# Optimization experiments

Hardware: AMD Instinct MI355X
Metric: run time of the kernel (lower is better)

## Reference

```python
import jax, jax.numpy as jnp
import numpy as np

N_LEADS = 12
N_HEADS = 4
LN_EPS = 1e-5

def _ecg_adj_norm():
    # Fixed 12-lead ECG adjacency with self loops, symmetric GCN normalization
    conns = [(0,1),(0,2),(1,2),(0,3),(1,3),(2,3),(0,4),(1,4),(1,5),(2,5),
             (6,7),(7,8),(8,9),(9,10),(10,11),(0,6),(1,9),(2,11)]
    A = np.zeros((N_LEADS, N_LEADS), dtype=np.float32)
    for i, j in conns:
        A[i, j] = 1.0
        A[j, i] = 1.0
    A += np.eye(N_LEADS, dtype=np.float32)
    d = A.sum(axis=1)
    dinv = 1.0 / np.sqrt(d)
    return jnp.asarray(dinv[:, None] * A * dinv[None, :])  # [12,12]

A_NORM = _ecg_adj_norm()

def gcn(x, W, b):
    # x: [B,12,F] -> A_norm @ (x W) + b
    return jnp.einsum('ij,bjf->bif', A_NORM, x @ W) + b

def mha(x, in_w, in_b, out_w, out_b):
    # x: [B,S,E]; torch nn.MultiheadAttention, batch_first=True
    B, S, E = x.shape
    D = E // N_HEADS
    qkv = x @ in_w.T + in_b                      # [B,S,3E]
    q, k, v = jnp.split(qkv, 3, axis=-1)
    def heads(t):
        return t.reshape(B, S, N_HEADS, D).transpose(0, 2, 1, 3)  # [B,H,S,D]
    q, k, v = heads(q), heads(k), heads(v)
    scores = jnp.einsum('bhsd,bhtd->bhst', q, k) / jnp.sqrt(jnp.float32(D))
    attn = jax.nn.softmax(scores, axis=-1)
    o = jnp.einsum('bhst,bhtd->bhsd', attn, v)   # [B,H,S,D]
    o = o.transpose(0, 2, 1, 3).reshape(B, S, E)
    return o @ out_w.T + out_b

def layer_norm(x, g, b):
    mu = x.mean(axis=-1, keepdims=True)
    var = ((x - mu) ** 2).mean(axis=-1, keepdims=True)
    return (x - mu) * jax.lax.rsqrt(var + LN_EPS) * g + b

def setup_inputs() -> dict:
    key = jax.random.key(0)
    ks = jax.random.split(key, 8)
    B, F_IN, H, OUT = 8192, 512, 256, 256
    s = lambda fan: 1.0 / np.sqrt(fan)
    return {
        'x': jax.random.normal(ks[0], (B, N_LEADS, F_IN), dtype=jnp.float32),
        'W1': jax.random.normal(ks[1], (F_IN, H), dtype=jnp.float32) * s(F_IN),
        'b1': jnp.zeros((H,), jnp.float32),
        'W2': jax.random.normal(ks[2], (H, H), dtype=jnp.float32) * s(H),
        'b2': jnp.zeros((H,), jnp.float32),
        'W3': jax.random.normal(ks[3], (H, OUT), dtype=jnp.float32) * s(H),
        'b3': jnp.zeros((OUT,), jnp.float32),
        'in_proj_w': jax.random.normal(ks[4], (3 * H, H), dtype=jnp.float32) * s(H),
        'in_proj_b': jnp.zeros((3 * H,), jnp.float32),
        'out_proj_w': jax.random.normal(ks[5], (H, H), dtype=jnp.float32) * s(H),
        'out_proj_b': jnp.zeros((H,), jnp.float32),
        'ln_g': jnp.ones((H,), jnp.float32),
        'ln_b': jnp.zeros((H,), jnp.float32),
    }

def reference(x, W1, b1, W2, b2, W3, b3, in_proj_w, in_proj_b, out_proj_w, out_proj_b, ln_g, ln_b):
    h = jax.nn.relu(gcn(x, W1, b1))              # dropout is identity at eval
    h = jax.nn.relu(gcn(h, W2, b2))              # [B,12,H]
    att = mha(h, in_proj_w, in_proj_b, out_proj_w, out_proj_b)
    h = layer_norm(h + att, ln_g, ln_b)
    h3 = gcn(h, W3, b3)                          # [B,12,OUT]
    w = jax.nn.softmax(h3.mean(axis=-1), axis=1) # [B,12] attention pooling
    x_weighted = jnp.einsum('bno,bn->bo', h3, w)
    x_max = h3.max(axis=1)
    return jnp.concatenate([x_weighted, x_max], axis=1)  # [B, 2*OUT]
```

## Files before the change

### kernel.cpp

```cpp
#include <hip/hip_runtime.h>
#include <hip/hip_bf16.h>
#include <cstdint>
#include <cstddef>

typedef unsigned short u16;
typedef u16 u16x8 __attribute__((ext_vector_type(8)));
typedef u16 u16x4 __attribute__((ext_vector_type(4)));
typedef __bf16 bf16x8 __attribute__((ext_vector_type(8)));
typedef float f32x4 __attribute__((ext_vector_type(4)));

__device__ const unsigned short ADJ_MASK[12] = {
    95u, 575u, 2095u, 15u, 19u, 38u, 193u, 448u, 896u, 1794u, 3584u, 3076u};

__device__ __forceinline__ float b2f(u16 u) {
  union { unsigned int i; float f; } v;
  v.i = ((unsigned int)u) << 16;
  return v.f;
}
__device__ __forceinline__ u16 f2b(float f) {
  union { float f; unsigned int i; } v;
  v.f = f;
  unsigned int r = v.i + 0x7fffu + ((v.i >> 16) & 1u);
  return (u16)(r >> 16);
}

__device__ __forceinline__ void build_anorm(float* An) {
  int t = threadIdx.x;
  if (t < 144) {
    int i = t / 12, j = t % 12;
    float di = (float)__popc((int)ADJ_MASK[i]);
    float dj = (float)__popc((int)ADJ_MASK[j]);
    An[t] = ((ADJ_MASK[i] >> j) & 1) ? (1.0f / sqrtf(di * dj)) : 0.0f;
  }
}

__global__ void __launch_bounds__(256) k_detect2(const void* a, const void* b,
                                                 int* flags) {
  const unsigned int* w = (const unsigned int*)(blockIdx.x ? b : a);
  __shared__ int s;
  if (threadIdx.x == 0) s = 0;
  __syncthreads();
  int cnt = 0;
  for (int t = 0; t < 16; ++t) {
    unsigned int v = w[t * 256 + threadIdx.x];
    unsigned int e = (v >> 7) & 0xFFu;
    if (e != 0u && (e < 0x5Au || e > 0x89u)) ++cnt;
  }
  atomicAdd(&s, cnt);
  __syncthreads();
  if (threadIdx.x == 0) flags[blockIdx.x] = (s > 1024) ? 1 : 0;
}

__global__ void __launch_bounds__(256) k_cvt_small(
    const void* b1, const void* b2, const void* b3, const void* inb,
    const void* outb, const void* lng, const void* lnb, u16* dst,
    const int* flag) {
  int idx = blockIdx.x * 256 + threadIdx.x;
  if (idx >= 2304) return;
  const void* src;
  int off = idx;
  if (idx < 256)       { src = b1; }
  else if (idx < 512)  { src = b2;   off = idx - 256; }
  else if (idx < 768)  { src = b3;   off = idx - 512; }
  else if (idx < 1536) { src = inb;  off = idx - 768; }
  else if (idx < 1792) { src = outb; off = idx - 1536; }
  else if (idx < 2048) { src = lng;  off = idx - 1792; }
  else                 { src = lnb;  off = idx - 2048; }
  dst[idx] = (*flag) ? f2b(((const float*)src)[off]) : ((const u16*)src)[off];
}

__global__ void __launch_bounds__(256) k_cvt_w(const void* inw,
                                               const void* outw, u16* dst,
                                               const int* flag) {
  int idx = blockIdx.x * 256 + threadIdx.x;
  const void* src = (idx < 196608) ? inw : outw;
  int off = (idx < 196608) ? idx : idx - 196608;
  dst[idx] = (*flag) ? f2b(((const float*)src)[off]) : ((const u16*)src)[off];
}

__global__ void __launch_bounds__(256) k_transpose3(const void* W1,
                                                    const void* W2,
                                                    const void* W3, u16* dst,
                                                    const int* flag) {
  int idx = blockIdx.x * 256 + threadIdx.x;
  const void* src;
  int R, C, li = idx;
  if (idx < 131072)      { src = W1; R = 512; C = 256; }
  else if (idx < 196608) { src = W2; R = 256; C = 256; li = idx - 131072; }
  else                   { src = W3; R = 256; C = 256; li = idx - 196608; }
  int c = li / R, r = li - c * R;
  u16 v = (*flag) ? f2b(((const float*)src)[r * C + c])
                  : ((const u16*)src)[r * C + c];
  dst[(idx - li) + c * R + r] = v;
}

__global__ void __launch_bounds__(256) k_mix(const u16* __restrict__ in,
                                             const u16* __restrict__ bias,
                                             u16* __restrict__ out, int relu) {
  __shared__ u16 X[6144];
  __shared__ float An[144];
  build_anorm(An);
  const int tid = threadIdx.x;
  const long base = (long)blockIdx.x * 6144;
#pragma unroll
  for (int i = 0; i < 3; ++i) {
    int idx = i * 256 + tid;
    *(u16x8*)(X + idx * 8) = *(const u16x8*)(in + base + idx * 8);
  }
  __syncthreads();
#pragma unroll
  for (int v = 0; v < 3; ++v) {
    int idx = v * 256 + tid;
    int s = idx / 384;
    int rem = idx - s * 384;
    int i = rem >> 5;
    int fg = rem & 31;
    float a[8];
#pragma unroll
    for (int u = 0; u < 8; ++u) a[u] = b2f(bias[fg * 8 + u]);
    for (int j = 0; j < 12; ++j) {
      float c = An[i * 12 + j];
      if (c != 0.0f) {
        u16x8 y = *(const u16x8*)(X + (s * 12 + j) * 256 + fg * 8);
#pragma unroll
        for (int u = 0; u < 8; ++u) a[u] += c * b2f(y[u]);
      }
    }
    u16x8 o;
#pragma unroll
    for (int u = 0; u < 8; ++u) {
      float vv = relu ? fmaxf(a[u], 0.0f) : a[u];
      o[u] = f2b(vv);
    }
    *(u16x8*)(out + base + idx * 8) = o;
  }
}

__device__ __forceinline__ void gemm_core(const void* __restrict__ A, int lda,
                                          int isf32,
                                          const u16* __restrict__ Bt,
                                          u16* As, u16* Bs,
                                          long m0, long n0, int K,
                                          f32x4 acc[6][4]) {
  const int tid = threadIdx.x;
  const int wave = tid >> 6, lane = tid & 63;
  const int q = lane >> 4, r16 = lane & 15;
  f32x4 zero = {0.f, 0.f, 0.f, 0.f};
#pragma unroll
  for (int a = 0; a < 6; ++a)
#pragma unroll
    for (int b = 0; b < 4; ++b) acc[a][b] = zero;

  for (int k0 = 0; k0 < K; k0 += 64) {
    if (isf32) {
      const float* Af = (const float*)A;
#pragma unroll
      for (int i = 0; i < 3; ++i) {
        int idx = i * 256 + tid;
        int rr = idx >> 3, cg = idx & 7;
        const float* sp = Af + (m0 + rr) * (long)lda + k0 + cg * 8;
        u16x8 t;
#pragma unroll
        for (int u = 0; u < 8; ++u) t[u] = f2b(sp[u]);
        *(u16x8*)(As + rr * 72 + cg * 8) = t;
      }
    } else {
      const u16* Ab = (const u16*)A;
#pragma unroll
      for (int i = 0; i < 3; ++i) {
        int idx = i * 256 + tid;
        int rr = idx >> 3, cg = idx & 7;
        *(u16x8*)(As + rr * 72 + cg * 8) =
            *(const u16x8*)(Ab + (m0 + rr) * (long)lda + k0 + cg * 8);
      }
    }
#pragma unroll
    for (int i = 0; i < 8; ++i) {
      int idx = i * 256 + tid;
      int rr = idx >> 3, cg = idx & 7;
      *(u16x8*)(Bs + rr * 72 + cg * 8) =
          *(const u16x8*)(Bt + (n0 + rr) * (long)K + k0 + cg * 8);
    }
    __syncthreads();
#pragma unroll
    for (int ks = 0; ks < 64; ks += 32) {
      bf16x8 af[6], bfv[4];
#pragma unroll
      for (int rb = 0; rb < 6; ++rb)
        af[rb] = *(const bf16x8*)(As + (rb * 16 + r16) * 72 + ks + q * 8);
#pragma unroll
      for (int cb = 0; cb < 4; ++cb)
        bfv[cb] = *(const bf16x8*)(Bs + ((wave * 4 + cb) * 16 + r16) * 72 + ks + q * 8);
#pragma unroll
      for (int rb = 0; rb < 6; ++rb)
#pragma unroll
        for (int cb = 0; cb < 4; ++cb)
          acc[rb][cb] = __builtin_amdgcn_mfma_f32_16x16x32_bf16(
              af[rb], bfv[cb], acc[rb][cb], 0, 0, 0);
    }
    __syncthreads();
  }
}

template <bool BIAS>
__global__ void __launch_bounds__(256, 2) k_gemm(const void* __restrict__ A,
                                                 int lda,
                                                 const u16* __restrict__ Bt,
                                                 const u16* __restrict__ bias,
                                                 u16* __restrict__ C,
                                                 int K, int Ntot,
                                                 const int* aflag) {
  __shared__ u16 As[96 * 72];
  __shared__ u16 Bs[256 * 72];
  f32x4 acc[6][4];
  const long m0 = (long)blockIdx.x * 96;
  const long n0 = (long)blockIdx.y * 256;
  int isf32 = aflag ? *aflag : 0;
  gemm_core(A, lda, isf32, Bt, As, Bs, m0, n0, K, acc);
  const int tid = threadIdx.x;
  const int wave = tid >> 6, lane = tid & 63;
  const int q = lane >> 4, r16 = lane & 15;
#pragma unroll
  for (int cb = 0; cb < 4; ++cb) {
    long col = n0 + (wave * 4 + cb) * 16 + r16;
    float bvv = BIAS ? b2f(bias[col]) : 0.0f;
#pragma unroll
    for (int rb = 0; rb < 6; ++rb) {
#pragma unroll
      for (int rr = 0; rr < 4; ++rr) {
        long row = m0 + rb * 16 + q * 4 + rr;
        C[row * (long)Ntot + col] = f2b(acc[rb][cb][rr] + bvv);
      }
    }
  }
}

__global__ void __launch_bounds__(256) k_attn(u16* __restrict__ QKV) {
  __shared__ u16 T[12 * 768];
  __shared__ float Sc[4][12][12];
  const int tid = threadIdx.x;
  const long base = (long)blockIdx.x * (12 * 768);
#pragma unroll
  for (int i = 0; i < 9; ++i) {
    int idx = i * 256 + tid;
    *(u16x4*)(T + idx * 4) = *(const u16x4*)(QKV + base + idx * 4);
  }
  __syncthreads();
  for (int p = tid; p < 576; p += 256) {
    int h = p / 144, r = p % 144, i = r / 12, j = r % 12;
    const u16* qp = T + i * 768 + h * 64;
    const u16* kp = T + j * 768 + 256 + h * 64;
    float s = 0.f;
#pragma unroll
    for (int dv = 0; dv < 8; ++dv) {
      u16x8 qv = *(const u16x8*)(qp + dv * 8);
      u16x8 kv = *(const u16x8*)(kp + dv * 8);
#pragma unroll
      for (int u = 0; u < 8; ++u) s += b2f(qv[u]) * b2f(kv[u]);
    }
    Sc[h][i][j] = s * 0.125f;
  }
  __syncthreads();
  if (tid < 48) {
    int h = tid / 12, i = tid % 12;
    float m = -1e30f;
#pragma unroll
    for (int j = 0; j < 12; ++j) m = fmaxf(m, Sc[h][i][j]);
    float e[12];
    float ssum = 0.f;
#pragma unroll
    for (int j = 0; j < 12; ++j) {
      e[j] = __expf(Sc[h][i][j] - m);
      ssum += e[j];
    }
    float inv = 1.0f / ssum;
#pragma unroll
    for (int j = 0; j < 12; ++j) Sc[h][i][j] = e[j] * inv;
  }
  __syncthreads();
  {
    int h = tid >> 6;
    int d = tid & 63;
    float vv[12];
#pragma unroll
    for (int j = 0; j < 12; ++j) vv[j] = b2f(T[j * 768 + 512 + h * 64 + d]);
#pragma unroll
    for (int i = 0; i < 12; ++i) {
      float o = 0.f;
#pragma unroll
      for (int j = 0; j < 12; ++j) o += Sc[h][i][j] * vv[j];
      QKV[base + i * 768 + h * 64 + d] = f2b(o);
    }
  }
}

__global__ void __launch_bounds__(256) k_resid_ln_mix(
    const u16* __restrict__ H, const u16* __restrict__ Oa,
    const u16* __restrict__ g, const u16* __restrict__ bb,
    u16* __restrict__ out) {
  __shared__ float Xn[12 * 256];
  __shared__ float An[144];
  __shared__ float mu[12], rs[12];
  build_anorm(An);
  const int tid = threadIdx.x;
  const long baseH = (long)blockIdx.x * 3072;
  const long baseO = (long)blockIdx.x * 9216;
#pragma unroll
  for (int i = 0; i < 3; ++i) {
    int idx = i * 256 + tid;
    int row = idx >> 6, c4 = idx & 63;
    u16x4 hv = *(const u16x4*)(H + baseH + idx * 4);
    u16x4 ov = *(const u16x4*)(Oa + baseO + row * 768 + c4 * 4);
#pragma unroll
    for (int u = 0; u < 4; ++u) Xn[idx * 4 + u] = b2f(hv[u]) + b2f(ov[u]);
  }
  __syncthreads();
  {
    int wave = tid >> 6, lane = tid & 63;
    for (int rr = wave; rr < 12; rr += 4) {
      float s = 0.f, s2 = 0.f;
#pragma unroll
      for (int u = 0; u < 4; ++u) {
        float xv = Xn[rr * 256 + u * 64 + lane];
        s += xv;
        s2 += xv * xv;
      }
#pragma unroll
      for (int off = 32; off > 0; off >>= 1) {
        s += __shfl_down(s, off, 64);
        s2 += __shfl_down(s2, off, 64);
      }
      if (lane == 0) {
        float m = s * (1.0f / 256.0f);
        float var = s2 * (1.0f / 256.0f) - m * m;
        mu[rr] = m;
        rs[rr] = rsqrtf(var + 1e-5f);
      }
    }
  }
  __syncthreads();
  {
    float gv = b2f(g[tid]);
    float bv = b2f(bb[tid]);
    float xn[12];
#pragma unroll
    for (int i = 0; i < 12; ++i) {
      float x = Xn[i * 256 + tid];
      xn[i] = (x - mu[i]) * rs[i] * gv + bv;
    }
#pragma unroll
    for (int i = 0; i < 12; ++i) {
      float o = 0.f;
#pragma unroll
      for (int j = 0; j < 12; ++j) o += An[i * 12 + j] * xn[j];
      out[baseH + i * 256 + tid] = f2b(o);
    }
  }
}

__global__ void __launch_bounds__(256) k_attn_mega(
    u16* __restrict__ H, const u16* __restrict__ inw,
    const u16* __restrict__ inb, const u16* __restrict__ outw,
    const u16* __restrict__ outb, const u16* __restrict__ lng,
    const u16* __restrict__ lnb) {
  __shared__ u16 Hs[32 * 264];
  __shared__ u16 Qs[32 * 264];
  __shared__ u16 KVs[24 * 512];
  __shared__ float Sc[4][2][12][12];
  __shared__ float An[144];
  __shared__ float mu[24], rs[24];
  const int tid = threadIdx.x;
  const int wave = tid >> 6, lane = tid & 63;
  const int q = lane >> 4, r16 = lane & 15;
  build_anorm(An);
  const long base = (long)blockIdx.x * 6144;
#pragma unroll
  for (int i = 0; i < 3; ++i) {
    int idx = i * 256 + tid;
    int rr = idx >> 5, cg = idx & 31;
    *(u16x8*)(Hs + rr * 264 + cg * 8) = *(const u16x8*)(H + base + idx * 8);
  }
  {
    int rr = 24 + (tid >> 5), cg = tid & 31;
    u16x8 z = {0, 0, 0, 0, 0, 0, 0, 0};
    *(u16x8*)(Hs + rr * 264 + cg * 8) = z;
  }
  __syncthreads();
  {
    f32x4 acc[2][12];
    f32x4 zero = {0.f, 0.f, 0.f, 0.f};
#pragma unroll
    for (int rb = 0; rb < 2; ++rb)
#pragma unroll
      for (int c = 0; c < 12; ++c) acc[rb][c] = zero;
    for (int k0 = 0; k0 < 256; k0 += 32) {
      bf16x8 af[2];
#pragma unroll
      for (int rb = 0; rb < 2; ++rb)
        af[rb] = *(const bf16x8*)(Hs + (rb * 16 + r16) * 264 + k0 + q * 8);
#pragma unroll
      for (int c = 0; c < 12; ++c) {
        bf16x8 bf = *(const bf16x8*)(inw + (long)((wave * 12 + c) * 16 + r16) * 256 + k0 + q * 8);
#pragma unroll
        for (int rb = 0; rb < 2; ++rb)
          acc[rb][c] = __builtin_amdgcn_mfma_f32_16x16x32_bf16(af[rb], bf, acc[rb][c], 0, 0, 0);
      }
    }
#pragma unroll
    for (int c = 0; c < 12; ++c) {
      int col = (wave * 12 + c) * 16 + r16;
      float bv = b2f(inb[col]);
#pragma unroll
      for (int rb = 0; rb < 2; ++rb)
#pragma unroll
        for (int rr2 = 0; rr2 < 4; ++rr2) {
          int row = rb * 16 + q * 4 + rr2;
          float v = acc[rb][c][rr2] + bv;
          if (col < 256) Qs[row * 264 + col] = f2b(v);
          else if (row < 24) KVs[row * 512 + col - 256] = f2b(v);
        }
    }
  }
  __syncthreads();
  {
    int h = wave;
#pragma unroll
    for (int t = 0; t < 5; ++t) {
      int p = t * 64 + lane;
      if (p < 288) {
        int s = p / 144, r = p - s * 144, i = r / 12, j = r - i * 12;
        const u16* qp = Qs + (s * 12 + i) * 264 + h * 64;
        const u16* kp = KVs + (s * 12 + j) * 512 + h * 64;
        float dot = 0.f;
#pragma unroll
        for (int dv = 0; dv < 8; ++dv) {
          u16x8 qv = *(const u16x8*)(qp + dv * 8);
          u16x8 kv = *(const u16x8*)(kp + dv * 8);
#pragma unroll
          for (int u = 0; u < 8; ++u) dot += b2f(qv[u]) * b2f(kv[u]);
        }
        Sc[h][s][i][j] = dot * 0.125f;
      }
    }
  }
  __syncthreads();
  if (lane < 24) {
    int h = wave, s = lane / 12, i = lane - (lane / 12) * 12;
    float m = -1e30f;
#pragma unroll
    for (int j = 0; j < 12; ++j) m = fmaxf(m, Sc[h][s][i][j]);
    float e[12];
    float ssum = 0.f;
#pragma unroll
    for (int j = 0; j < 12; ++j) {
      e[j] = __expf(Sc[h][s][i][j] - m);
      ssum += e[j];
    }
    float inv = 1.0f / ssum;
#pragma unroll
    for (int j = 0; j < 12; ++j) Sc[h][s][i][j] = e[j] * inv;
  }
  __syncthreads();
  {
    int h = wave, d = lane;
    for (int si = 0; si < 24; ++si) {
      int s = si / 12;
      float o = 0.f;
#pragma unroll
      for (int j = 0; j < 12; ++j)
        o += Sc[h][s][si - s * 12][j] * b2f(KVs[(s * 12 + j) * 512 + 256 + h * 64 + d]);
      Qs[si * 264 + h * 64 + d] = f2b(o);
    }
  }
  __syncthreads();
  {
    f32x4 acc[2][4];
    f32x4 zero = {0.f, 0.f, 0.f, 0.f};
#pragma unroll
    for (int rb = 0; rb < 2; ++rb)
#pragma unroll
      for (int cb = 0; cb < 4; ++cb) acc[rb][cb] = zero;
    for (int k0 = 0; k0 < 256; k0 += 32) {
      bf16x8 af[2];
#pragma unroll
      for (int rb = 0; rb < 2; ++rb)
        af[rb] = *(const bf16x8*)(Qs + (rb * 16 + r16) * 264 + k0 + q * 8);
#pragma unroll
      for (int cb = 0; cb < 4; ++cb) {
        bf16x8 bf = *(const bf16x8*)(outw + (long)((wave * 4 + cb) * 16 + r16) * 256 + k0 + q * 8);
#pragma unroll
        for (int rb = 0; rb < 2; ++rb)
          acc[rb][cb] = __builtin_amdgcn_mfma_f32_16x16x32_bf16(af[rb], bf, acc[rb][cb], 0, 0, 0);
      }
    }
#pragma unroll
    for (int cb = 0; cb < 4; ++cb) {
      int col = (wave * 4 + cb) * 16 + r16;
      float ob = b2f(outb[col]);
#pragma unroll
      for (int rb = 0; rb < 2; ++rb)
#pragma unroll
        for (int rr2 = 0; rr2 < 4; ++rr2) {
          int row = rb * 16 + q * 4 + rr2;
          if (row < 24) {
            float x = acc[rb][cb][rr2] + ob + b2f(Hs[row * 264 + col]);
            Hs[row * 264 + col] = f2b(x);
          }
        }
    }
  }
  __syncthreads();
  {
    for (int rr2 = wave * 6; rr2 < wave * 6 + 6; ++rr2) {
      float s1 = 0.f, s2 = 0.f;
#pragma unroll
      for (int u = 0; u < 4; ++u) {
        float xv = b2f(Hs[rr2 * 264 + u * 64 + lane]);
        s1 += xv;
        s2 += xv * xv;
      }
#pragma unroll
      for (int off = 32; off > 0; off >>= 1) {
        s1 += __shfl_down(s1, off, 64);
        s2 += __shfl_down(s2, off, 64);
      }
      if (lane == 0) {
        float m = s1 * (1.0f / 256.0f);
        mu[rr2] = m;
        rs[rr2] = rsqrtf(s2 * (1.0f / 256.0f) - m * m + 1e-5f);
      }
    }
  }
  __syncthreads();
  {
    float gvv = b2f(lng[tid]);
    float bvv = b2f(lnb[tid]);
#pragma unroll
    for (int s = 0; s < 2; ++s) {
      float xn[12];
#pragma unroll
      for (int j = 0; j < 12; ++j) {
        int row = s * 12 + j;
        xn[j] = (b2f(Hs[row * 264 + tid]) - mu[row]) * rs[row] * gvv + bvv;
      }
#pragma unroll
      for (int i = 0; i < 12; ++i) {
        float o = 0.f;
#pragma unroll
        for (int j = 0; j < 12; ++j) o += An[i * 12 + j] * xn[j];
        H[base + (s * 12 + i) * 256 + tid] = f2b(o);
      }
    }
  }
}

__global__ void __launch_bounds__(256, 2) k_gemm_pool(const u16* __restrict__ A,
                                                      const u16* __restrict__ Bt,
                                                      const u16* __restrict__ bias,
                                                      float* __restrict__ out) {
  __shared__ __align__(16) char smraw[50688];
  __shared__ float rowsum[96];
  __shared__ float wsm[96];
  u16* As = (u16*)smraw;
  u16* Bs = As + 96 * 72;
  u16* Y = (u16*)smraw;
  f32x4 acc[6][4];
  const long m0 = (long)blockIdx.x * 96;
  gemm_core(A, 256, 0, Bt, As, Bs, m0, 0, 256, acc);
  const int tid = threadIdx.x;
  const int wave = tid >> 6, lane = tid & 63;
  const int q = lane >> 4, r16 = lane & 15;
#pragma unroll
  for (int cb = 0; cb < 4; ++cb) {
    int col = (wave * 4 + cb) * 16 + r16;
    float bvv = b2f(bias[col]);
#pragma unroll
    for (int rb = 0; rb < 6; ++rb)
#pragma unroll
      for (int rr = 0; rr < 4; ++rr) {
        int row = rb * 16 + q * 4 + rr;
        Y[row * 264 + col] = f2b(acc[rb][cb][rr] + bvv);
      }
  }
  __syncthreads();
  for (int row = wave; row < 96; row += 4) {
    float s = 0.f;
#pragma unroll
    for (int u = 0; u < 4; ++u) s += b2f(Y[row * 264 + u * 64 + lane]);
#pragma unroll
    for (int off = 32; off > 0; off >>= 1) s += __shfl_down(s, off, 64);
    if (lane == 0) rowsum[row] = s;
  }
  __syncthreads();
  if (tid < 8) {
    float m = -1e30f;
#pragma unroll
    for (int l = 0; l < 12; ++l) m = fmaxf(m, rowsum[tid * 12 + l]);
    float e[12];
    float ssum = 0.f;
#pragma unroll
    for (int l = 0; l < 12; ++l) {
      e[l] = __expf((rowsum[tid * 12 + l] - m) * (1.0f / 256.0f));
      ssum += e[l];
    }
    float inv = 1.0f / ssum;
#pragma unroll
    for (int l = 0; l < 12; ++l) wsm[tid * 12 + l] = e[l] * inv;
  }
  __syncthreads();
  {
    int s = tid >> 5, cg = tid & 31;
    float wa[8], mx[8];
#pragma unroll
    for (int u = 0; u < 8; ++u) {
      wa[u] = 0.f;
      mx[u] = -1e30f;
    }
#pragma unroll
    for (int l = 0; l < 12; ++l) {
      float w = wsm[s * 12 + l];
      u16x8 yv = *(const u16x8*)(Y + (s * 12 + l) * 264 + cg * 8);
#pragma unroll
      for (int u = 0; u < 8; ++u) {
        float y = b2f(yv[u]);
        wa[u] += w * y;
        mx[u] = fmaxf(mx[u], y);
      }
    }
    long ob = ((long)blockIdx.x * 8 + s) * 512;
#pragma unroll
    for (int u = 0; u < 8; ++u) {
      out[ob + cg * 8 + u] = wa[u];
      out[ob + 256 + cg * 8 + u] = mx[u];
    }
  }
}

extern "C" void kernel_launch(void* const* d_in, const int* in_sizes, int n_in,
                              void* d_out, int out_size, void* d_ws,
                              size_t ws_size, hipStream_t stream) {
  (void)in_sizes; (void)n_in; (void)out_size;
  const void* x    = d_in[0];
  const void* W1   = d_in[1];
  const void* b1   = d_in[2];
  const void* W2   = d_in[3];
  const void* b2   = d_in[4];
  const void* W3   = d_in[5];
  const void* b3   = d_in[6];
  const void* inw  = d_in[7];
  const void* inb  = d_in[8];
  const void* outw = d_in[9];
  const void* outb = d_in[10];
  const void* lng  = d_in[11];
  const void* lnb  = d_in[12];
  float* out = (float*)d_out;

  u16* ws16 = (u16*)d_ws;
  int* flags = (int*)d_ws;
  u16* W1T    = ws16 + 64;
  u16* W2T    = W1T + 131072;
  u16* W3T    = W2T + 65536;
  u16* inw_b  = W3T + 65536;
  u16* outw_b = inw_b + 196608;
  u16* b1b    = outw_b + 65536;
  u16* b2b    = b1b + 256;
  u16* b3b    = b2b + 256;
  u16* inbb   = b3b + 256;
  u16* outbb  = inbb + 768;
  u16* lngb   = outbb + 256;
  u16* lnbb   = lngb + 256;
  u16* BUF    = lnbb + 256;
  u16* QKV    = BUF + 25165824L;
  const size_t NEED_A = (size_t)(QKV + 75497472L - ws16) * 2;

  k_detect2<<<2, 256, 0, stream>>>(x, W1, flags);

  k_cvt_small<<<9, 256, 0, stream>>>(b1, b2, b3, inb, outb, lng, lnb, b1b,
                                     flags + 1);
  k_cvt_w<<<1024, 256, 0, stream>>>(inw, outw, inw_b, flags + 1);
  k_transpose3<<<1024, 256, 0, stream>>>(W1, W2, W3, W1T, flags + 1);

  k_gemm<false><<<dim3(1024, 1), 256, 0, stream>>>(x, 512, W1T, nullptr, BUF, 512, 256, flags);
  k_mix<<<4096, 256, 0, stream>>>(BUF, b1b, BUF, 1);
  k_gemm<false><<<dim3(1024, 1), 256, 0, stream>>>(BUF, 256, W2T, nullptr, BUF, 256, 256, nullptr);
  k_mix<<<4096, 256, 0, stream>>>(BUF, b2b, BUF, 1);

  if (ws_size >= NEED_A) {
    k_gemm<true><<<dim3(1024, 3), 256, 0, stream>>>(BUF, 256, inw_b, inbb, QKV, 256, 768, nullptr);
    k_attn<<<8192, 256, 0, stream>>>(QKV);
    k_gemm<true><<<dim3(1024, 1), 256, 0, stream>>>(QKV, 768, outw_b, outbb, QKV + 256, 256, 768, nullptr);
    k_resid_ln_mix<<<8192, 256, 0, stream>>>(BUF, QKV + 256, lngb, lnbb, BUF);
  } else {
    k_attn_mega<<<4096, 256, 0, stream>>>(BUF, inw_b, inbb, outw_b, outbb, lngb, lnbb);
  }
  k_gemm_pool<<<1024, 256, 0, stream>>>(BUF, W3T, b3b, out);
}
```

Baseline: 688.5 us.

## Load GEMM tiles directly into LDS with XOR-swizzled layout

Replaces the register-staged global-to-LDS copies of the bf16 A and B tiles with direct global_load_lds transfers of 16 bytes per lane. The padded 72-element row stride becomes an unpadded 64-element row with XOR swizzling of 16-byte chunks to avoid bank conflicts, and the fragment reads are updated to match. This removes the VGPR round trip and shrinks LDS use. The f32 input path still goes through registers, and correctness depends on the hardware support for 16-byte direct LDS loads and on the swizzle matching between writer and reader.

```diff
diff --git a/kernel.cpp b/kernel.cpp
--- a/kernel.cpp
+++ b/kernel.cpp
@@ -23,6 +23,11 @@
   unsigned int r = v.i + 0x7fffu + ((v.i >> 16) & 1u);
   return (u16)(r >> 16);
 }
+
+#define GLOAD_LDS16(gsrc, ldst)                                         \
+  __builtin_amdgcn_global_load_lds(                                     \
+      (const __attribute__((address_space(1))) unsigned int*)(gsrc),    \
+      (__attribute__((address_space(3))) unsigned int*)(ldst), 16, 0, 0)
 
 __device__ __forceinline__ void build_anorm(float* An) {
   int t = threadIdx.x;
@@ -162,35 +167,40 @@
         u16x8 t;
 #pragma unroll
         for (int u = 0; u < 8; ++u) t[u] = f2b(sp[u]);
-        *(u16x8*)(As + rr * 72 + cg * 8) = t;
+        *(u16x8*)(As + rr * 64 + ((cg ^ (rr & 7)) << 3)) = t;
       }
     } else {
       const u16* Ab = (const u16*)A;
 #pragma unroll
       for (int i = 0; i < 3; ++i) {
-        int idx = i * 256 + tid;
-        int rr = idx >> 3, cg = idx & 7;
-        *(u16x8*)(As + rr * 72 + cg * 8) =
-            *(const u16x8*)(Ab + (m0 + rr) * (long)lda + k0 + cg * 8);
+        int c = i * 256 + tid;
+        int rr = c >> 3, s = c & 7;
+        GLOAD_LDS16(Ab + (m0 + rr) * (long)lda + k0 + ((s ^ (rr & 7)) << 3),
+                    As + c * 8);
       }
     }
 #pragma unroll
     for (int i = 0; i < 8; ++i) {
-      int idx = i * 256 + tid;
-      int rr = idx >> 3, cg = idx & 7;
-      *(u16x8*)(Bs + rr * 72 + cg * 8) =
-          *(const u16x8*)(Bt + (n0 + rr) * (long)K + k0 + cg * 8);
+      int c = i * 256 + tid;
+      int rr = c >> 3, s = c & 7;
+      GLOAD_LDS16(Bt + (n0 + rr) * (long)K + k0 + ((s ^ (rr & 7)) << 3),
+                  Bs + c * 8);
     }
     __syncthreads();
 #pragma unroll
     for (int ks = 0; ks < 64; ks += 32) {
+      const int ck = q + (ks >> 3);
       bf16x8 af[6], bfv[4];
 #pragma unroll
-      for (int rb = 0; rb < 6; ++rb)
-        af[rb] = *(const bf16x8*)(As + (rb * 16 + r16) * 72 + ks + q * 8);
-#pragma unroll
-      for (int cb = 0; cb < 4; ++cb)
-        bfv[cb] = *(const bf16x8*)(Bs + ((wave * 4 + cb) * 16 + r16) * 72 + ks + q * 8);
+      for (int rb = 0; rb < 6; ++rb) {
+        int row = rb * 16 + r16;
+        af[rb] = *(const bf16x8*)(As + row * 64 + ((ck ^ (row & 7)) << 3));
+      }
+#pragma unroll
+      for (int cb = 0; cb < 4; ++cb) {
+        int row = (wave * 4 + cb) * 16 + r16;
+        bfv[cb] = *(const bf16x8*)(Bs + row * 64 + ((ck ^ (row & 7)) << 3));
+      }
 #pragma unroll
       for (int rb = 0; rb < 6; ++rb)
 #pragma unroll
@@ -210,8 +220,8 @@
                                                  u16* __restrict__ C,
                                                  int K, int Ntot,
                                                  const int* aflag) {
-  __shared__ u16 As[96 * 72];
-  __shared__ u16 Bs[256 * 72];
+  __shared__ u16 As[96 * 64];
+  __shared__ u16 Bs[256 * 64];
   f32x4 acc[6][4];
   const long m0 = (long)blockIdx.x * 96;
   const long n0 = (long)blockIdx.y * 256;
@@ -562,7 +572,7 @@
   __shared__ float rowsum[96];
   __shared__ float wsm[96];
   u16* As = (u16*)smraw;
-  u16* Bs = As + 96 * 72;
+  u16* Bs = As + 96 * 64;
   u16* Y = (u16*)smraw;
   f32x4 acc[6][4];
   const long m0 = (long)blockIdx.x * 96;
```

Result: faster. 652.2 us (-5.3%).
